# Performance work log

Measured on AMD Instinct MI355X. Metric: run time of the kernel, lower is better.

Reference implementation:

```python
import jax, jax.numpy as jnp
import numpy as np

IN_CH = 128
OUT_CH = 128
N_NODES = 20000
N_EDGES = 320000
EPS = 1e-5


def setup_inputs() -> dict:
    key = jax.random.key(0)
    ks = jax.random.split(key, 8)
    node_embeddings = jax.random.normal(ks[0], (N_NODES, IN_CH), dtype=jnp.float32)
    edge_index = jax.random.randint(ks[1], (2, N_EDGES), 0, N_NODES, dtype=jnp.int64)
    s = 1.0 / np.sqrt(IN_CH)
    W1 = jax.random.uniform(ks[2], (IN_CH, IN_CH), jnp.float32, -s, s)
    b1 = jax.random.uniform(ks[3], (IN_CH,), jnp.float32, -s, s)
    W2 = jax.random.uniform(ks[4], (IN_CH, IN_CH), jnp.float32, -s, s)
    b2 = jax.random.uniform(ks[5], (IN_CH,), jnp.float32, -s, s)
    sm = 1.0 / np.sqrt(2 * IN_CH)
    Wm = jax.random.uniform(ks[6], (2 * IN_CH, 2 * OUT_CH), jnp.float32, -sm, sm)
    bm = jax.random.uniform(ks[7], (2 * OUT_CH,), jnp.float32, -sm, sm)
    gamma = jnp.ones((OUT_CH,), jnp.float32)
    beta = jnp.zeros((OUT_CH,), jnp.float32)
    return {"node_embeddings": node_embeddings, "edge_index": edge_index,
            "W1": W1, "b1": b1, "W2": W2, "b2": b2,
            "Wm": Wm, "bm": bm, "gamma": gamma, "beta": beta}


def reference(node_embeddings, edge_index, W1, b1, W2, b2, Wm, bm, gamma, beta):
    # gather endpoint embeddings: [E, d]
    src = node_embeddings[edge_index[0]]
    dst = node_embeddings[edge_index[1]]
    src_emb = src @ W1 + b1                       # Linear v1
    dst_emb = dst @ W2 + b2                       # Linear v2
    edge_attr = jnp.concatenate([src_emb, dst_emb], axis=-1)  # [E, 2d]
    h = edge_attr @ Wm + bm                       # [E, 2*out]
    x, gate = jnp.split(h, 2, axis=-1)            # GeGLU (exact gelu, torch default)
    y = x * jax.nn.gelu(gate, approximate=False)  # [E, out]
    mu = jnp.mean(y, axis=-1, keepdims=True)
    var = jnp.var(y, axis=-1, keepdims=True)
    y_norm = (y - mu) * jax.lax.rsqrt(var + EPS)
    return y_norm * gamma + beta
```

## Files before the change

### kernel.cpp

```cpp
#include <hip/hip_runtime.h>
#include <hip/hip_fp16.h>
#include <math.h>


#define CH 128

typedef _Float16 half8 __attribute__((ext_vector_type(8)));
typedef float floatx4 __attribute__((ext_vector_type(4)));

__device__ __forceinline__ int permcol(int j2) {
  int c = j2 & 127;
  int isg = j2 >> 7;
  return ((c >> 1) << 2) | (isg << 1) | (c & 1);
}

__global__ __launch_bounds__(256) void prep_kernel(
    const float* __restrict__ W1, const float* __restrict__ b1,
    const float* __restrict__ W2, const float* __restrict__ b2,
    const float* __restrict__ Wm, const float* __restrict__ bm,
    __half* __restrict__ CcatT, float* __restrict__ dvec) {
  int bid = blockIdx.x;
  int tid = threadIdx.x;
  if (bid < 256) {
    int idx = bid * 256 + tid;
    int i = idx >> 9;
    int j = idx & 511;
    int jc = j & 255;
    const float* wrow = (j < 256) ? (W1 + i * CH) : (W2 + i * CH);
    const float* wm   = (j < 256) ? (Wm + jc) : (Wm + CH * 256 + jc);
    float acc = 0.f;
#pragma unroll 8
    for (int k = 0; k < CH; ++k) acc = fmaf(wrow[k], wm[k * 256], acc);
    int scol = (j & 256) | permcol(j & 255);
    CcatT[scol * CH + i] = __float2half(acc);
  } else if (tid < 256) {
    float acc = bm[tid];
#pragma unroll 8
    for (int k = 0; k < CH; ++k) {
      acc = fmaf(b1[k], Wm[k * 256 + tid], acc);
      acc = fmaf(b2[k], Wm[(CH + k) * 256 + tid], acc);
    }
    dvec[permcol(tid)] = acc;
  }
}

__global__ __launch_bounds__(256) void node_gemm(
    const float* __restrict__ A,
    const __half* __restrict__ BT,
    __half* __restrict__ C,
    int M) {
  __shared__ __align__(16) _Float16 As[64 * 136];
  __shared__ __align__(16) _Float16 Bs[64 * 136];
  const int tid = threadIdx.x;
  const int row0 = blockIdx.x * 64;
  const int col0 = blockIdx.y * 64;

#pragma unroll
  for (int rnd = 0; rnd < 4; ++rnd) {
    int idx = (tid + rnd * 256) * 8;
    int r = idx >> 7, c = idx & 127;
    int rg = row0 + r; if (rg >= M) rg = M - 1;
    float4 v0 = *(const float4*)(A + (size_t)rg * CH + c);
    float4 v1 = *(const float4*)(A + (size_t)rg * CH + c + 4);
    __half2 h0 = __floats2half2_rn(v0.x, v0.y);
    __half2 h1 = __floats2half2_rn(v0.z, v0.w);
    __half2 h2 = __floats2half2_rn(v1.x, v1.y);
    __half2 h3 = __floats2half2_rn(v1.z, v1.w);
    uint4 u;
    u.x = *(const unsigned int*)&h0; u.y = *(const unsigned int*)&h1;
    u.z = *(const unsigned int*)&h2; u.w = *(const unsigned int*)&h3;
    *(uint4*)(As + r * 136 + c) = u;
    uint4 w4 = *(const uint4*)(BT + (size_t)(col0 + r) * CH + c);
    *(uint4*)(Bs + r * 136 + c) = w4;
  }
  __syncthreads();

  const int w = tid >> 6, l = tid & 63;
  const int mr = w * 16 + (l & 15);
  const int kq = (l >> 4) * 8;

  half8 a[4];
#pragma unroll
  for (int kc = 0; kc < 4; ++kc)
    a[kc] = *(const half8*)(As + mr * 136 + kc * 32 + kq);

  floatx4 acc[4] = {{0,0,0,0},{0,0,0,0},{0,0,0,0},{0,0,0,0}};
#pragma unroll
  for (int kc = 0; kc < 4; ++kc) {
#pragma unroll
    for (int nb = 0; nb < 4; ++nb) {
      half8 b = *(const half8*)(Bs + (nb * 16 + (l & 15)) * 136 + kc * 32 + kq);
      acc[nb] = __builtin_amdgcn_mfma_f32_16x16x32_f16(a[kc], b, acc[nb], 0, 0, 0);
    }
  }

  const int colb = col0 + (l & 15);
  const int rowb = row0 + w * 16 + (l >> 4) * 4;
#pragma unroll
  for (int nb = 0; nb < 4; ++nb) {
#pragma unroll
    for (int rg = 0; rg < 4; ++rg) {
      int row = rowb + rg;
      if (row < M)
        C[(size_t)row * 512 + colb + nb * 16] = __float2half(acc[nb][rg]);
    }
  }
}

__device__ __forceinline__ float gelu_t(float g) {
  float g2 = g * g;
  float t = g * fmaf(g2, 0.10294515f, 2.3021858f);
  float u = exp2f(t);
  return g * u * __builtin_amdgcn_rcpf(1.0f + u);
}

__device__ __forceinline__ void process_edge(
    uint4 pu, uint4 qu, float4 dv0, float4 dv1, float4 gm, float4 bt,
    float* __restrict__ outp, int hl) {
  float2 px01 = __half22float2(*(const __half2*)&pu.x);
  float2 pg01 = __half22float2(*(const __half2*)&pu.y);
  float2 px23 = __half22float2(*(const __half2*)&pu.z);
  float2 pg23 = __half22float2(*(const __half2*)&pu.w);
  float2 qx01 = __half22float2(*(const __half2*)&qu.x);
  float2 qg01 = __half22float2(*(const __half2*)&qu.y);
  float2 qx23 = __half22float2(*(const __half2*)&qu.z);
  float2 qg23 = __half22float2(*(const __half2*)&qu.w);

  float x0 = px01.x + qx01.x + dv0.x;
  float x1 = px01.y + qx01.y + dv0.y;
  float g0 = pg01.x + qg01.x + dv0.z;
  float g1 = pg01.y + qg01.y + dv0.w;
  float x2 = px23.x + qx23.x + dv1.x;
  float x3 = px23.y + qx23.y + dv1.y;
  float g2 = pg23.x + qg23.x + dv1.z;
  float g3 = pg23.y + qg23.y + dv1.w;

  float y0 = x0 * gelu_t(g0);
  float y1 = x1 * gelu_t(g1);
  float y2 = x2 * gelu_t(g2);
  float y3 = x3 * gelu_t(g3);

  float s1 = (y0 + y1) + (y2 + y3);
  float s2 = fmaf(y0, y0, fmaf(y1, y1, fmaf(y2, y2, y3 * y3)));
#pragma unroll
  for (int off = 16; off; off >>= 1) {
    s1 += __shfl_xor(s1, off, 64);
    s2 += __shfl_xor(s2, off, 64);
  }
  float mu  = s1 * (1.0f / 128.0f);
  float var = s2 * (1.0f / 128.0f) - mu * mu;
  float rstd = rsqrtf(var + 1e-5f);

  float4 o;
  o.x = fmaf((y0 - mu) * rstd, gm.x, bt.x);
  o.y = fmaf((y1 - mu) * rstd, gm.y, bt.y);
  o.z = fmaf((y2 - mu) * rstd, gm.z, bt.z);
  o.w = fmaf((y3 - mu) * rstd, gm.w, bt.w);
  *(float4*)(outp + hl * 4) = o;
}

__global__ __launch_bounds__(256) void edge_kernel(
    const __half* __restrict__ PQ,
    const float* __restrict__ dvec,
    const float* __restrict__ gamma,
    const float* __restrict__ beta,
    const int* __restrict__ eidx,
    float* __restrict__ out,
    int E) {
  const int wave = threadIdx.x >> 6;
  const int lane = threadIdx.x & 63;
  const int hl = lane & 31;
  const int side = lane >> 5;
  const int eA = blockIdx.x * 16 + wave * 4 + side;
  const int eB = eA + 2;
  if (eA >= E) return;
  const bool vB = (eB < E);

  float4 dv0 = *(const float4*)(dvec + hl * 8);
  float4 dv1 = *(const float4*)(dvec + hl * 8 + 4);
  float4 gm  = *(const float4*)(gamma + hl * 4);
  float4 bt  = *(const float4*)(beta + hl * 4);

  const int sA = eidx[eA],           dA = eidx[E + eA];
  const int sB = vB ? eidx[eB] : 0,  dB = vB ? eidx[E + eB] : 0;

  const char* pqb = (const char*)PQ;
  uint4 puA = *(const uint4*)(pqb + (size_t)sA * 1024 + hl * 16);
  uint4 quA = *(const uint4*)(pqb + (size_t)dA * 1024 + 512 + hl * 16);
  uint4 puB = *(const uint4*)(pqb + (size_t)sB * 1024 + hl * 16);
  uint4 quB = *(const uint4*)(pqb + (size_t)dB * 1024 + 512 + hl * 16);

  process_edge(puA, quA, dv0, dv1, gm, bt, out + (size_t)eA * CH, hl);
  if (vB)
    process_edge(puB, quB, dv0, dv1, gm, bt, out + (size_t)eB * CH, hl);
}

extern "C" void kernel_launch(void* const* d_in, const int* in_sizes, int n_in,
                              void* d_out, int out_size, void* d_ws, size_t ws_size,
                              hipStream_t stream) {
  const float* emb   = (const float*)d_in[0];
  const int*   eidx  = (const int*)d_in[1];
  const float* W1    = (const float*)d_in[2];
  const float* b1    = (const float*)d_in[3];
  const float* W2    = (const float*)d_in[4];
  const float* b2    = (const float*)d_in[5];
  const float* Wm    = (const float*)d_in[6];
  const float* bm    = (const float*)d_in[7];
  const float* gamma = (const float*)d_in[8];
  const float* beta  = (const float*)d_in[9];

  const int M = in_sizes[0] / CH;
  const int E = in_sizes[1] / 2;

  float*  dvec  = (float*)d_ws;
  __half* CcatT = (__half*)(dvec + 256);
  __half* PQ    = CcatT + 512 * CH;

  prep_kernel<<<257, 256, 0, stream>>>(W1, b1, W2, b2, Wm, bm, CcatT, dvec);

  dim3 g2((M + 63) / 64, 512 / 64);
  node_gemm<<<g2, 256, 0, stream>>>(emb, CcatT, PQ, M);

  edge_kernel<<<(E + 15) / 16, 256, 0, stream>>>(PQ, dvec, gamma, beta, eidx,
                                                 (float*)d_out, E);
}
```

Baseline: 94.61 us.

## Bucket edges by source node range and remap edge blocks for L2 locality

Adds a scatter kernel that partitions edges into 32 buckets by source-node range, using per-block atomics into preallocated fixed-capacity buckets. The edge kernel then walks the bucketed order, and its blocks are interleaved so that each of 8 groups of blocks, likely one per XCD, covers a contiguous range of buckets. The aim is better cache reuse of the PQ rows gathered for source nodes. The cost is an extra pass over edge_index plus extra reads of the sorted arrays. Each bucket holds at most 11264 edges, which is only safe when sources are roughly uniform, and output writes become scattered.

```diff
diff --git a/kernel.cpp b/kernel.cpp
--- a/kernel.cpp
+++ b/kernel.cpp
@@ -4,6 +4,8 @@
 
 
 #define CH 128
+#define NB 32
+#define BCAP 11264
 
 typedef _Float16 half8 __attribute__((ext_vector_type(8)));
 typedef float floatx4 __attribute__((ext_vector_type(4)));
@@ -18,7 +20,8 @@
     const float* __restrict__ W1, const float* __restrict__ b1,
     const float* __restrict__ W2, const float* __restrict__ b2,
     const float* __restrict__ Wm, const float* __restrict__ bm,
-    __half* __restrict__ CcatT, float* __restrict__ dvec) {
+    __half* __restrict__ CcatT, float* __restrict__ dvec,
+    unsigned int* __restrict__ cursor) {
   int bid = blockIdx.x;
   int tid = threadIdx.x;
   if (bid < 256) {
@@ -34,6 +37,7 @@
     int scol = (j & 256) | permcol(j & 255);
     CcatT[scol * CH + i] = __float2half(acc);
   } else if (tid < 256) {
+    if (tid < NB) cursor[tid] = (unsigned int)tid * BCAP;
     float acc = bm[tid];
 #pragma unroll 8
     for (int k = 0; k < CH; ++k) {
@@ -41,6 +45,41 @@
       acc = fmaf(b2[k], Wm[(CH + k) * 256 + tid], acc);
     }
     dvec[permcol(tid)] = acc;
+  }
+}
+
+#define SCHUNK 2048
+__global__ __launch_bounds__(256) void scatter_kernel(
+    const int* __restrict__ eidx, int E, int npb,
+    unsigned int* __restrict__ cursor,
+    int* __restrict__ sorted_e, int2* __restrict__ sorted_sd) {
+  __shared__ unsigned int lcnt[NB], lbase[NB], loff[NB];
+  __shared__ signed char lkey[SCHUNK];
+  const int tid = threadIdx.x;
+  const int c0 = blockIdx.x * SCHUNK;
+  if (tid < NB) { lcnt[tid] = 0; loff[tid] = 0; }
+  __syncthreads();
+  for (int i = tid; i < SCHUNK; i += 256) {
+    int e = c0 + i;
+    int k = -1;
+    if (e < E) { int s = eidx[e]; k = s / npb; atomicAdd(&lcnt[k], 1u); }
+    lkey[i] = (signed char)k;
+  }
+  __syncthreads();
+  if (tid < NB) {
+    unsigned int c = lcnt[tid];
+    lbase[tid] = c ? atomicAdd(&cursor[tid], c) : 0u;
+  }
+  __syncthreads();
+  for (int i = tid; i < SCHUNK; i += 256) {
+    int e = c0 + i;
+    if (e < E) {
+      int k = (int)lkey[i];
+      unsigned int r = atomicAdd(&loff[k], 1u);
+      unsigned int pos = lbase[k] + r;
+      sorted_e[pos] = e;
+      sorted_sd[pos] = make_int2(eidx[e], eidx[E + e]);
+    }
   }
 }
 
@@ -164,25 +203,32 @@
     const float* __restrict__ dvec,
     const float* __restrict__ gamma,
     const float* __restrict__ beta,
-    const int* __restrict__ eidx,
-    float* __restrict__ out,
-    int E) {
+    const unsigned int* __restrict__ cursor,
+    const int* __restrict__ sorted_e,
+    const int2* __restrict__ sorted_sd,
+    float* __restrict__ out) {
+  const int per = gridDim.x >> 3;
+  const int nb2 = (blockIdx.x & 7) * per + (blockIdx.x >> 3);
   const int wave = threadIdx.x >> 6;
   const int lane = threadIdx.x & 63;
   const int hl = lane & 31;
   const int side = lane >> 5;
-  const int eA = blockIdx.x * 16 + wave * 4 + side;
-  const int eB = eA + 2;
-  if (eA >= E) return;
-  const bool vB = (eB < E);
+  const int i0 = nb2 * 16 + wave * 4 + side;
+
+  const int slotA = i0, slotB = i0 + 2;
+  const int bA = slotA / BCAP, bB = slotB / BCAP;
+  const bool vA = (unsigned int)slotA < cursor[bA];
+  const bool vB = (unsigned int)slotB < cursor[bB];
+  if (!vA && !vB) return;
 
   float4 dv0 = *(const float4*)(dvec + hl * 8);
   float4 dv1 = *(const float4*)(dvec + hl * 8 + 4);
   float4 gm  = *(const float4*)(gamma + hl * 4);
   float4 bt  = *(const float4*)(beta + hl * 4);
 
-  const int sA = eidx[eA],           dA = eidx[E + eA];
-  const int sB = vB ? eidx[eB] : 0,  dB = vB ? eidx[E + eB] : 0;
+  int eA = 0, sA = 0, dA = 0, eB = 0, sB = 0, dB = 0;
+  if (vA) { eA = sorted_e[slotA]; int2 sd = sorted_sd[slotA]; sA = sd.x; dA = sd.y; }
+  if (vB) { eB = sorted_e[slotB]; int2 sd = sorted_sd[slotB]; sB = sd.x; dB = sd.y; }
 
   const char* pqb = (const char*)PQ;
   uint4 puA = *(const uint4*)(pqb + (size_t)sA * 1024 + hl * 16);
@@ -190,7 +236,8 @@
   uint4 puB = *(const uint4*)(pqb + (size_t)sB * 1024 + hl * 16);
   uint4 quB = *(const uint4*)(pqb + (size_t)dB * 1024 + 512 + hl * 16);
 
-  process_edge(puA, quA, dv0, dv1, gm, bt, out + (size_t)eA * CH, hl);
+  if (vA)
+    process_edge(puA, quA, dv0, dv1, gm, bt, out + (size_t)eA * CH, hl);
   if (vB)
     process_edge(puB, quB, dv0, dv1, gm, bt, out + (size_t)eB * CH, hl);
 }
@@ -211,16 +258,26 @@
 
   const int M = in_sizes[0] / CH;
   const int E = in_sizes[1] / 2;
-
-  float*  dvec  = (float*)d_ws;
-  __half* CcatT = (__half*)(dvec + 256);
-  __half* PQ    = CcatT + 512 * CH;
-
-  prep_kernel<<<257, 256, 0, stream>>>(W1, b1, W2, b2, Wm, bm, CcatT, dvec);
+  const int npb = (M + NB - 1) / NB;
+
+  float*        dvec      = (float*)d_ws;
+  unsigned int* cursor    = (unsigned int*)(dvec + 256);
+  __half*       CcatT     = (__half*)(cursor + 64);
+  int*          sorted_e  = (int*)(CcatT + 512 * CH);
+  int2*         sorted_sd = (int2*)(sorted_e + NB * BCAP);
+  __half*       PQ        = (__half*)(sorted_sd + NB * BCAP);
+
+  prep_kernel<<<257, 256, 0, stream>>>(W1, b1, W2, b2, Wm, bm, CcatT, dvec,
+                                       cursor);
+
+  scatter_kernel<<<(E + SCHUNK - 1) / SCHUNK, 256, 0, stream>>>(
+      eidx, E, npb, cursor, sorted_e, sorted_sd);
 
   dim3 g2((M + 63) / 64, 512 / 64);
   node_gemm<<<g2, 256, 0, stream>>>(emb, CcatT, PQ, M);
 
-  edge_kernel<<<(E + 15) / 16, 256, 0, stream>>>(PQ, dvec, gamma, beta, eidx,
-                                                 (float*)d_out, E);
-}
+  const int nslots = NB * BCAP;
+  edge_kernel<<<nslots / 16, 256, 0, stream>>>(PQ, dvec, gamma, beta, cursor,
+                                               sorted_e, sorted_sd,
+                                               (float*)d_out);
+}
```

After: 93.07 us. No clear change (-1.6%).
